# Kernel optimization log

Measured on AMD Instinct MI355X. Metric: run time of the kernel, lower is better.

Reference implementation:

```python
import jax, jax.numpy as jnp
import numpy as np

FRACTION_BITS = 16
INTEGER_BITS = 16


def round_to_fixed(x):
    # floor-quantize to 2^-16 steps, clamp to signed 16-bit integer range
    delta = 2.0 ** (-FRACTION_BITS)
    bound = 2.0 ** (INTEGER_BITS - 1)
    return jnp.clip(jnp.floor(x / delta) * delta, -bound, bound - 1.0)


def setup_inputs() -> dict:
    key = jax.random.key(0)
    k1, k2, k3, k4 = jax.random.split(key, 4)
    N, IN_F, OUT_F = 4096, 4096, 4096
    inp = jax.random.normal(k1, (N, IN_F), dtype=jnp.float32)
    # reset_parameters: shift ~ U(-10,-1), sign ~ U(-1,0), bias ~ U(-b,b), b=1/sqrt(fan_in)
    shift = jax.random.uniform(k2, (OUT_F, IN_F), minval=-10.0, maxval=-1.0, dtype=jnp.float32)
    sign = jax.random.uniform(k3, (OUT_F, IN_F), minval=-1.0, maxval=0.0, dtype=jnp.float32)
    b = 1.0 / np.sqrt(IN_F)
    bias = jax.random.uniform(k4, (OUT_F,), minval=-b, maxval=b, dtype=jnp.float32)
    return {"input": inp, "shift": shift, "sign": sign, "bias": bias}


def reference(input, shift, sign, bias):
    # eager (non-kernel) path of LinearShiftFunction.forward
    q_in = round_to_fixed(input)
    q_bias = round_to_fixed(bias)
    s = jnp.clip(sign, -1.0, 1.0)
    v = jnp.exp2(jnp.round(shift)) * jnp.sign(s)  # [out_f, in_f] power-of-two weights
    out = q_in @ v.T + q_bias[None, :]
    return out
```

## Files before the change

kernel.cpp:

```cpp
#include <hip/hip_runtime.h>
#include <hip/hip_bf16.h>


#define BM 256
#define BN 256
#define BK 64

typedef __bf16 bf16_t;
typedef __attribute__((ext_vector_type(8))) __bf16 bf16x8;
typedef __attribute__((ext_vector_type(4))) __bf16 bf16x4;
typedef __attribute__((ext_vector_type(4))) float f32x4;

__device__ __forceinline__ float q16(float x) {
    float f = floorf(x * 65536.0f) * (1.0f / 65536.0f);
    return fminf(fmaxf(f, -32768.0f), 32767.0f);
}

__global__ void quant_input_kernel(const float* __restrict__ in,
                                   bf16_t* __restrict__ out, int nvec) {
    int stride = gridDim.x * blockDim.x;
    for (int i = blockIdx.x * blockDim.x + threadIdx.x; i < nvec; i += stride) {
        float4 v = reinterpret_cast<const float4*>(in)[i];
        bf16x4 o;
        o[0] = (bf16_t)q16(v.x);
        o[1] = (bf16_t)q16(v.y);
        o[2] = (bf16_t)q16(v.z);
        o[3] = (bf16_t)q16(v.w);
        reinterpret_cast<bf16x4*>(out)[i] = o;
    }
}

__global__ void make_weight_kernel(const float* __restrict__ shift,
                                   const float* __restrict__ sign_,
                                   bf16_t* __restrict__ out, int nvec) {
    int stride = gridDim.x * blockDim.x;
    for (int i = blockIdx.x * blockDim.x + threadIdx.x; i < nvec; i += stride) {
        float4 sh = reinterpret_cast<const float4*>(shift)[i];
        float4 sg = reinterpret_cast<const float4*>(sign_)[i];
        float shs[4] = {sh.x, sh.y, sh.z, sh.w};
        float sgs[4] = {sg.x, sg.y, sg.z, sg.w};
        bf16x4 o;
#pragma unroll
        for (int j = 0; j < 4; ++j) {
            float s = fminf(fmaxf(sgs[j], -1.0f), 1.0f);
            float sv = (s > 0.0f) ? 1.0f : ((s < 0.0f) ? -1.0f : 0.0f);
            o[j] = (bf16_t)(exp2f(rintf(shs[j])) * sv);
        }
        reinterpret_cast<bf16x4*>(out)[i] = o;
    }
}


#define VMW(N) asm volatile("s_waitcnt vmcnt(" #N ")" ::: "memory")
#define BARF() do { __builtin_amdgcn_s_barrier(); asm volatile("" ::: "memory"); } while (0)

#define STAGE(LDSOFF, SRC) do {                                                          \
    const bf16_t* _s = (SRC);                                                            \
    bf16_t* _d = &lds[(LDSOFF)] + tid * 8;                                               \
    __builtin_amdgcn_global_load_lds((const __attribute__((address_space(1))) void*)_s,  \
                                     (__attribute__((address_space(3))) void*)_d,        \
                                     16, 0, 0);                                          \
    __builtin_amdgcn_global_load_lds(                                                    \
        (const __attribute__((address_space(1))) void*)(_s + (size_t)64 * K),            \
        (__attribute__((address_space(3))) void*)(_d + 4096), 16, 0, 0);                 \
} while (0)

#define READ_A(BUF, MH) do {                                                             \
    const bf16_t* _As = &lds[(BUF) * 32768 + wm * 8192];                                 \
    _Pragma("unroll") for (int m = 0; m < 4; ++m)                                        \
        _Pragma("unroll") for (int kk = 0; kk < 2; ++kk)                                 \
            af[m][kk] = *(const bf16x8*)&_As[((MH) * 64 + m * 16 + fr) * 64 +            \
                                             ((((kk << 2) | hi) ^ fr7) << 3)];           \
} while (0)

#define READ_B(BUF, NH, BF) do {                                                         \
    const bf16_t* _Bs = &lds[(BUF) * 32768 + 16384 + (wn >> 1) * 8192];                  \
    _Pragma("unroll") for (int n = 0; n < 2; ++n)                                        \
        _Pragma("unroll") for (int kk = 0; kk < 2; ++kk)                                 \
            BF[n][kk] = *(const bf16x8*)&_Bs[((wn & 1) * 64 + ((NH) * 2 + n) * 16 + fr)  \
                                                 * 64 +                                  \
                                             ((((kk << 2) | hi) ^ fr7) << 3)];           \
} while (0)

#define QUAD(MH, NH, BF) do {                                                            \
    _Pragma("unroll") for (int m = 0; m < 4; ++m)                                        \
        _Pragma("unroll") for (int n = 0; n < 2; ++n)                                    \
            _Pragma("unroll") for (int kk = 0; kk < 2; ++kk)                             \
                acc[(MH) * 4 + m][(NH) * 2 + n] =                                        \
                    __builtin_amdgcn_mfma_f32_16x16x32_bf16(                             \
                        af[m][kk], BF[n][kk], acc[(MH) * 4 + m][(NH) * 2 + n], 0, 0, 0); \
} while (0)

#define MFMA_PH(MH, NH, BF)                                                              \
    __builtin_amdgcn_s_setprio(1);                                                       \
    QUAD(MH, NH, BF);                                                                    \
    __builtin_amdgcn_s_setprio(0);

#define TILE(BUF, T, S01, S23, ENDW) do {                                                \
                                                                            \
    READ_A(BUF, 0);                                                                      \
    READ_B(BUF, 0, b0f);                                                                 \
    if (S01) STAGE(((BUF) ^ 1) * 32768 + 3 * 8192, srcB1 + (size_t)((T) + 1) * 64);      \
    MFMA_PH(0, 0, b0f)                                                                   \
                                                                            \
    READ_B(BUF, 1, b1f);                                                                 \
    if (S01) STAGE(((BUF) ^ 1) * 32768 + 1 * 8192, srcA1 + (size_t)((T) + 1) * 64);      \
    MFMA_PH(0, 1, b1f)                                                                   \
    BARF();                                                      \
                                                                            \
    READ_A(BUF, 1);                                                                      \
    if (S23) STAGE((BUF) * 32768 + 2 * 8192, srcB0 + (size_t)((T) + 2) * 64);            \
    MFMA_PH(1, 0, b0f)                                                                   \
                                          \
    if (S23) STAGE((BUF) * 32768 + 0 * 8192, srcA0 + (size_t)((T) + 2) * 64);            \
    MFMA_PH(1, 1, b1f)                                                                   \
    if ((ENDW) == 4) VMW(4);                                                             \
    else if ((ENDW) == 0) VMW(0);                                                        \
    BARF();                                                           \
} while (0)

__global__ __launch_bounds__(512, 2)
void gemm256_kernel(const bf16_t* __restrict__ A,
                    const bf16_t* __restrict__ B,
                    const float* __restrict__ bias,
                    float* __restrict__ C,
                    int M, int N, int K) {
    __shared__ bf16_t lds[65536];

    const int ntn = N / BN;
    const int nwg = gridDim.x;
    const int q = nwg >> 3, r = nwg & 7;
    const int xcd = blockIdx.x & 7, lid = blockIdx.x >> 3;
    const int swz = (xcd < r ? xcd * (q + 1) : r * (q + 1) + (xcd - r) * q) + lid;
    const int tile_m = (swz / ntn) * BM;
    const int tile_n = (swz % ntn) * BN;

    const int tid = threadIdx.x;
    const int lane = tid & 63;
    const int wid = tid >> 6;
    const int wm = wid >> 2;
    const int wn = wid & 3;
    const int fr = lane & 15;
    const int hi = lane >> 4;
    const int fr7 = fr & 7;

    const int colsrc_e = ((((tid & 7) * 16) ^ ((tid & 56) << 1)) >> 1);
    const bf16_t* srcA0 = A + (size_t)(tile_m + (tid >> 3)) * K + colsrc_e;
    const bf16_t* srcA1 = srcA0 + (size_t)128 * K;
    const bf16_t* srcB0 = B + (size_t)(tile_n + (tid >> 3)) * K + colsrc_e;
    const bf16_t* srcB1 = srcB0 + (size_t)128 * K;

    bf16x8 af[4][2], b0f[2][2], b1f[2][2];
    f32x4 acc[8][4] = {};

    STAGE(16384, srcB0);
    STAGE(0, srcA0);
    STAGE(24576, srcB1);
    STAGE(8192, srcA1);
    STAGE(32768 + 16384, srcB0 + 64);
    STAGE(32768 + 0, srcA0 + 64);
    VMW(4);
    BARF();

    const int npairs = K / 128;
    for (int i = 0; i < npairs - 1; ++i) {
        TILE(0, 2 * i, 1, 1, 4);
        TILE(1, 2 * i + 1, 1, 1, 4);
    }
    TILE(0, 2 * npairs - 2, 1, 0, 0);
    TILE(1, 2 * npairs - 1, 0, 0, -1);

    float qb[4];
#pragma unroll
    for (int ng = 0; ng < 4; ++ng)
        qb[ng] = q16(bias[tile_n + wn * 64 + ng * 16 + fr]);
#pragma unroll
    for (int mg = 0; mg < 8; ++mg) {
        const int grow0 = tile_m + wm * 128 + mg * 16 + hi * 4;
#pragma unroll
        for (int ng = 0; ng < 4; ++ng) {
            const int gcol = tile_n + wn * 64 + ng * 16 + fr;
#pragma unroll
            for (int rr = 0; rr < 4; ++rr)
                C[(size_t)(grow0 + rr) * N + gcol] = acc[mg][ng][rr] + qb[ng];
        }
    }
}

extern "C" void kernel_launch(void* const* d_in, const int* in_sizes, int n_in,
                              void* d_out, int out_size, void* d_ws, size_t ws_size,
                              hipStream_t stream) {
    const float* inp   = (const float*)d_in[0];
    const float* shift = (const float*)d_in[1];
    const float* sign_ = (const float*)d_in[2];
    const float* bias  = (const float*)d_in[3];
    float* out = (float*)d_out;

    const int OUT_F = in_sizes[3];
    const int IN_F  = in_sizes[1] / OUT_F;
    const int Mrows = in_sizes[0] / IN_F;

    bf16_t* Aq = (bf16_t*)d_ws;
    bf16_t* Wq = Aq + (size_t)Mrows * IN_F;

    const int nA = Mrows * IN_F;
    const int nW = OUT_F * IN_F;

    quant_input_kernel<<<2048, 256, 0, stream>>>(inp, Aq, nA >> 2);
    make_weight_kernel<<<2048, 256, 0, stream>>>(shift, sign_, Wq, nW >> 2);

    dim3 grid((Mrows / BM) * (OUT_F / BN));
    gemm256_kernel<<<grid, 512, 0, stream>>>(Aq, Wq, bias, out,
                                             Mrows, OUT_F, IN_F);
}
```

Before: 158.1 us.

## Load B fragments directly from global into registers and triple-buffer A in LDS

```diff
diff --git a/kernel.cpp b/kernel.cpp
--- a/kernel.cpp
+++ b/kernel.cpp
@@ -65,58 +65,49 @@
         (__attribute__((address_space(3))) void*)(_d + 4096), 16, 0, 0);                 \
 } while (0)
 
-#define READ_A(BUF, MH) do {                                                             \
-    const bf16_t* _As = &lds[(BUF) * 32768 + wm * 8192];                                 \
+#define STAGE_A(SLOT, T) do {                                                            \
+    STAGE((SLOT) * 16384 + 0,    srcA0 + (size_t)(T) * 64);                              \
+    STAGE((SLOT) * 16384 + 8192, srcA1 + (size_t)(T) * 64);                              \
+} while (0)
+
+#define READ_A8(AB, MH) do {                                                             \
     _Pragma("unroll") for (int m = 0; m < 4; ++m)                                        \
         _Pragma("unroll") for (int kk = 0; kk < 2; ++kk)                                 \
-            af[m][kk] = *(const bf16x8*)&_As[((MH) * 64 + m * 16 + fr) * 64 +            \
+            af[m][kk] = *(const bf16x8*)&(AB)[wm * 8192 +                                \
+                                             ((MH) * 64 + m * 16 + fr) * 64 +            \
                                              ((((kk << 2) | hi) ^ fr7) << 3)];           \
 } while (0)
 
-#define READ_B(BUF, NH, BF) do {                                                         \
-    const bf16_t* _Bs = &lds[(BUF) * 32768 + 16384 + (wn >> 1) * 8192];                  \
-    _Pragma("unroll") for (int n = 0; n < 2; ++n)                                        \
-        _Pragma("unroll") for (int kk = 0; kk < 2; ++kk)                                 \
-            BF[n][kk] = *(const bf16x8*)&_Bs[((wn & 1) * 64 + ((NH) * 2 + n) * 16 + fr)  \
-                                                 * 64 +                                  \
-                                             ((((kk << 2) | hi) ^ fr7) << 3)];           \
-} while (0)
-
-#define QUAD(MH, NH, BF) do {                                                            \
+#define LOADB(R, T) do {                                                                 \
+    _Pragma("unroll") for (int kk = 0; kk < 2; ++kk)                                     \
+        b[R][kk] = *(const bf16x8*)(gB##R + (size_t)(T) * 64 + kk * 32);                 \
+} while (0)
+
+#define MQUAD(MH, NH) do {                                                               \
+    __builtin_amdgcn_s_setprio(1);                                                       \
     _Pragma("unroll") for (int m = 0; m < 4; ++m)                                        \
         _Pragma("unroll") for (int n = 0; n < 2; ++n)                                    \
             _Pragma("unroll") for (int kk = 0; kk < 2; ++kk)                             \
                 acc[(MH) * 4 + m][(NH) * 2 + n] =                                        \
                     __builtin_amdgcn_mfma_f32_16x16x32_bf16(                             \
-                        af[m][kk], BF[n][kk], acc[(MH) * 4 + m][(NH) * 2 + n], 0, 0, 0); \
-} while (0)
-
-#define MFMA_PH(MH, NH, BF)                                                              \
-    __builtin_amdgcn_s_setprio(1);                                                       \
-    QUAD(MH, NH, BF);                                                                    \
-    __builtin_amdgcn_s_setprio(0);
-
-#define TILE(BUF, T, S01, S23, ENDW) do {                                                \
-                                                                            \
-    READ_A(BUF, 0);                                                                      \
-    READ_B(BUF, 0, b0f);                                                                 \
-    if (S01) STAGE(((BUF) ^ 1) * 32768 + 3 * 8192, srcB1 + (size_t)((T) + 1) * 64);      \
-    MFMA_PH(0, 0, b0f)                                                                   \
-                                                                            \
-    READ_B(BUF, 1, b1f);                                                                 \
-    if (S01) STAGE(((BUF) ^ 1) * 32768 + 1 * 8192, srcA1 + (size_t)((T) + 1) * 64);      \
-    MFMA_PH(0, 1, b1f)                                                                   \
-    BARF();                                                      \
-                                                                            \
-    READ_A(BUF, 1);                                                                      \
-    if (S23) STAGE((BUF) * 32768 + 2 * 8192, srcB0 + (size_t)((T) + 2) * 64);            \
-    MFMA_PH(1, 0, b0f)                                                                   \
-                                          \
-    if (S23) STAGE((BUF) * 32768 + 0 * 8192, srcA0 + (size_t)((T) + 2) * 64);            \
-    MFMA_PH(1, 1, b1f)                                                                   \
-    if ((ENDW) == 4) VMW(4);                                                             \
-    else if ((ENDW) == 0) VMW(0);                                                        \
-    BARF();                                                           \
+                        af[m][kk], b[(NH) * 2 + n][kk],                                  \
+                        acc[(MH) * 4 + m][(NH) * 2 + n], 0, 0, 0);                       \
+    __builtin_amdgcn_s_setprio(0);                                                       \
+} while (0)
+
+#define TILE(T, AB, S2, DO_B, DO_A, W) do {                                              \
+    READ_A8(AB, 0);                                                                      \
+    MQUAD(0, 0);                                                                         \
+    MQUAD(0, 1);                                                                         \
+    READ_A8(AB, 1);                                                                      \
+    MQUAD(1, 0);                                                                         \
+    if (DO_B) { LOADB(0, (T) + 1); LOADB(1, (T) + 1); }                                  \
+    MQUAD(1, 1);                                                                         \
+    if (DO_B) { LOADB(2, (T) + 1); LOADB(3, (T) + 1); }                                  \
+    if (DO_A) STAGE_A(S2, (T) + 2);                                                      \
+    if ((W) == 12) VMW(12);                                                              \
+    else if ((W) == 8) VMW(8);                                                           \
+    BARF();                                                                              \
 } while (0)
 
 __global__ __launch_bounds__(512, 2)
@@ -125,7 +116,7 @@
                     const float* __restrict__ bias,
                     float* __restrict__ C,
                     int M, int N, int K) {
-    __shared__ bf16_t lds[65536];
+    __shared__ bf16_t lds[49152];
 
     const int ntn = N / BN;
     const int nwg = gridDim.x;
@@ -147,28 +138,42 @@
     const int colsrc_e = ((((tid & 7) * 16) ^ ((tid & 56) << 1)) >> 1);
     const bf16_t* srcA0 = A + (size_t)(tile_m + (tid >> 3)) * K + colsrc_e;
     const bf16_t* srcA1 = srcA0 + (size_t)128 * K;
-    const bf16_t* srcB0 = B + (size_t)(tile_n + (tid >> 3)) * K + colsrc_e;
-    const bf16_t* srcB1 = srcB0 + (size_t)128 * K;
-
-    bf16x8 af[4][2], b0f[2][2], b1f[2][2];
+
+    const bf16_t* gB0 = B + (size_t)(tile_n + wn * 64 + 0 * 16 + fr) * K + hi * 8;
+    const bf16_t* gB1 = B + (size_t)(tile_n + wn * 64 + 1 * 16 + fr) * K + hi * 8;
+    const bf16_t* gB2 = B + (size_t)(tile_n + wn * 64 + 2 * 16 + fr) * K + hi * 8;
+    const bf16_t* gB3 = B + (size_t)(tile_n + wn * 64 + 3 * 16 + fr) * K + hi * 8;
+
+    bf16x8 af[4][2], b[4][2];
     f32x4 acc[8][4] = {};
 
-    STAGE(16384, srcB0);
-    STAGE(0, srcA0);
-    STAGE(24576, srcB1);
-    STAGE(8192, srcA1);
-    STAGE(32768 + 16384, srcB0 + 64);
-    STAGE(32768 + 0, srcA0 + 64);
-    VMW(4);
+    STAGE_A(0, 0);
+    STAGE_A(1, 1);
+    LOADB(0, 0); LOADB(1, 0); LOADB(2, 0); LOADB(3, 0);
+    VMW(12);
     BARF();
 
-    const int npairs = K / 128;
-    for (int i = 0; i < npairs - 1; ++i) {
-        TILE(0, 2 * i, 1, 1, 4);
-        TILE(1, 2 * i + 1, 1, 1, 4);
-    }
-    TILE(0, 2 * npairs - 2, 1, 0, 0);
-    TILE(1, 2 * npairs - 1, 0, 0, -1);
+    int scur = 0;
+    for (int t = 0; t < 62; ++t) {
+        const int s2 = scur >= 1 ? scur - 1 : scur + 2;
+        const bf16_t* ab = &lds[scur * 16384];
+        TILE(t, ab, s2, 1, 1, 12);
+        scur = scur >= 2 ? 0 : scur + 1;
+    }
+    {
+        const bf16_t* ab = &lds[scur * 16384];
+        TILE(62, ab, 0, 1, 0, 8);
+        scur = scur >= 2 ? 0 : scur + 1;
+    }
+    {
+        const bf16_t* ab = &lds[scur * 16384];
+        READ_A8(ab, 0);
+        MQUAD(0, 0);
+        MQUAD(0, 1);
+        READ_A8(ab, 1);
+        MQUAD(1, 0);
+        MQUAD(1, 1);
+    }
 
     float qb[4];
 #pragma unroll
```

After: 195.7 us. 1.24x slower.
